# Kernel tuning notes

Hardware: AMD Instinct MI355X
Metric: run time of the kernel (lower is better)

## Reference

```python
import jax, jax.numpy as jnp
import numpy as np
from math import comb

N_INPUT, N_HIDDEN, N_LATENT = 2, 1024, 16
T, B = 320, 192
DEG = N_LATENT // 2 - 1          # 7
NPTS = DEG + 1                   # 8 control points
LAT = N_LATENT + N_LATENT // 2   # 24

_COMB = jnp.array([comb(DEG, i) for i in range(NPTS)], dtype=jnp.float32)
_I = jnp.arange(NPTS, dtype=jnp.float32)


def setup_inputs() -> dict:
    key = jax.random.key(0)
    ks = jax.random.split(key, 24)
    H = N_HIDDEN
    w = lambda k, shape, sc: (jax.random.normal(k, shape, jnp.float32) * sc)
    return dict(
        x=jax.random.normal(ks[0], (T, B, N_INPUT), jnp.float32),
        latent_ctrlpt=jax.random.normal(ks[1], (B, N_LATENT), jnp.float32),
        latent_ratw=jax.random.uniform(ks[2], (B, N_LATENT // 2), jnp.float32, 0.1, 1.0),
        # h0/c0 projection linears (forward/backward directions)
        W_hf=w(ks[3], (H, LAT), 0.2), b_hf=jnp.zeros((H,), jnp.float32),
        W_hb=w(ks[4], (H, LAT), 0.2), b_hb=jnp.zeros((H,), jnp.float32),
        W_cf=w(ks[5], (H, LAT), 0.2), b_cf=jnp.zeros((H,), jnp.float32),
        W_cb=w(ks[6], (H, LAT), 0.2), b_cb=jnp.zeros((H,), jnp.float32),
        # bi-LSTM weights, PyTorch gate order (i, f, g, o)
        W_ih_f=w(ks[7], (4 * H, N_INPUT), 0.03), W_hh_f=w(ks[8], (4 * H, H), 0.03),
        b_ih_f=jnp.zeros((4 * H,), jnp.float32), b_hh_f=jnp.zeros((4 * H,), jnp.float32),
        W_ih_b=w(ks[9], (4 * H, N_INPUT), 0.03), W_hh_b=w(ks[10], (4 * H, H), 0.03),
        b_ih_b=jnp.zeros((4 * H,), jnp.float32), b_hh_b=jnp.zeros((4 * H,), jnp.float32),
        # t-logits head
        W_log=w(ks[11], (1, 2 * H), 0.03), b_log=jnp.zeros((1,), jnp.float32),
    )


def _lstm_dir(x_tm, h0, c0, W_ih, W_hh, b_ih, b_hh, reverse):
    # x_tm: (T, B, in). Precompute input projection once (compute-efficient).
    xs = jnp.einsum('tbi,gi->tbg', x_tm, W_ih) + b_ih + b_hh  # (T, B, 4H)

    def step(carry, xt):
        h, c = carry
        g = xt + h @ W_hh.T
        i, f, gg, o = jnp.split(g, 4, axis=-1)
        c = jax.nn.sigmoid(f) * c + jax.nn.sigmoid(i) * jnp.tanh(gg)
        h = jax.nn.sigmoid(o) * jnp.tanh(c)
        return (h, c), h

    _, hs = jax.lax.scan(step, (h0, c0), xs, reverse=reverse)
    return hs  # (T, B, H)


def reference(x, latent_ctrlpt, latent_ratw,
              W_hf, b_hf, W_hb, b_hb, W_cf, b_cf, W_cb, b_cb,
              W_ih_f, W_hh_f, b_ih_f, b_hh_f,
              W_ih_b, W_hh_b, b_ih_b, b_hh_b,
              W_log, b_log):
    latent = jnp.concatenate([latent_ctrlpt, latent_ratw], axis=1)  # (B, LAT)
    h0f = jnp.tanh(latent @ W_hf.T + b_hf)
    h0b = jnp.tanh(latent @ W_hb.T + b_hb)
    c0f = jnp.tanh(latent @ W_cf.T + b_cf)
    c0b = jnp.tanh(latent @ W_cb.T + b_cb)

    hf = _lstm_dir(x, h0f, c0f, W_ih_f, W_hh_f, b_ih_f, b_hh_f, reverse=False)
    hb = _lstm_dir(x, h0b, c0b, W_ih_b, W_hh_b, b_ih_b, b_hh_b, reverse=True)
    out = jnp.concatenate([hf, hb], axis=-1)           # (T, B, 2H)
    out = jnp.transpose(out, (1, 0, 2))                # batch_first (B, T, 2H)

    logits = (out @ W_log.T + b_log)[..., 0]           # (B, T)
    ts = jnp.cumsum(jax.nn.softmax(logits, axis=1), axis=1)  # (B, T) in (0, 1]

    P = latent_ctrlpt.reshape(-1, NPTS, 2)             # (B, NPTS, 2)
    r = latent_ratw.reshape(-1, NPTS)                  # (B, NPTS)

    # Rational Bezier curve, batched over B and T (replaces per-sample loop)
    t = ts[..., None]                                   # (B, T, 1)
    basis = _COMB * t ** _I * (1.0 - t) ** (DEG - _I)   # (B, T, NPTS)
    num = basis * r[:, None, :]
    w = num / num.sum(-1, keepdims=True)
    curves = jnp.einsum('btn,bnd->btd', w, P)           # (B, T, 2)

    # mean of squared consecutive control-point distances, averaged over batch
    d2 = ((P[:, 1:, :] - P[:, :-1, :]) ** 2).sum(-1)    # (B, NPTS-1)
    reg = d2.mean()
    return curves, reg
```

## Files before the change

### kernel.cpp

```cpp
#include <hip/hip_runtime.h>
#include <stdint.h>

#define T_STEPS 320
#define BATCH   192
#define HID     1024
#define NBLK    256

typedef unsigned short u16;
typedef __bf16 bf16x8 __attribute__((ext_vector_type(8)));
typedef float  f32x4  __attribute__((ext_vector_type(4)));
typedef unsigned int u32x4 __attribute__((ext_vector_type(4)));

#define OFF_BAR      0u
#define OFF_PART     4096u
#define MEMSET_BYTES 3936256u
#define OFF_C0       3936256u
#define OFF_H        5509120u
#define OFF_WPACK    7081984u
#define OFF_COEF     23859200u
#define WS_NEED      23990272u

#define DMP_WK_STRIDE 6528
#define DMP_BYTES     104448
#define DYN_LDS       104464

__device__ __forceinline__ u16 f2bf(float f) {
  unsigned u = __float_as_uint(f);
  unsigned r = (u + 0x7FFFu + ((u >> 16) & 1u)) >> 16;
  return (u16)r;
}
__device__ __forceinline__ float sigm(float x)   { return 1.f / (1.f + __expf(-x)); }
__device__ __forceinline__ float tanh_f(float x) { return 1.f - 2.f / (1.f + __expf(2.f * x)); }

__global__ void pack_k(const float* __restrict__ Whhf, const float* __restrict__ Whhb,
                       u16* __restrict__ wpack)
{
  int lin = blockIdx.x * 256 + threadIdx.x;
  int lane = lin & 63;
  int cg   = (lin >> 6) & 3;
  int ks   = (lin >> 8) & 31;
  int jsl  = (lin >> 13) & 63;
  int dir  = (lin >> 19) & 1;
  int col  = cg * 16 + (lane & 15);
  int R    = (col & 3) * 1024 + jsl * 16 + (col >> 2);
  int kb   = ks * 32 + (lane >> 4) * 8;
  const float* W = dir ? Whhb : Whhf;
  const float* src = W + (size_t)R * 1024 + kb;
  unsigned w[4];
  #pragma unroll
  for (int e = 0; e < 4; ++e) {
    unsigned lo = f2bf(src[2 * e]);
    unsigned hi = f2bf(src[2 * e + 1]);
    w[e] = lo | (hi << 16);
  }
  *((uint4*)(wpack + (size_t)lin * 8)) = make_uint4(w[0], w[1], w[2], w[3]);
}

__global__ void coef_k(const float* __restrict__ Wihf, const float* __restrict__ bihf,
                       const float* __restrict__ bhhf,
                       const float* __restrict__ Wihb, const float* __restrict__ bihb,
                       const float* __restrict__ bhhb, float* __restrict__ coef)
{
  int id  = blockIdx.x * 256 + threadIdx.x;
  int col = id & 63;
  int jsl = (id >> 6) & 63;
  int dir = (id >> 12) & 1;
  int R   = (col & 3) * 1024 + jsl * 16 + (col >> 2);
  const float* Wih = dir ? Wihb : Wihf;
  const float* bi  = dir ? bihb : bihf;
  const float* bh  = dir ? bhhb : bhhf;
  float4 v;
  v.x = Wih[(size_t)R * 2 + 0];
  v.y = Wih[(size_t)R * 2 + 1];
  v.z = bi[R] + bh[R];
  v.w = 0.f;
  ((float4*)coef)[id] = v;
}

__global__ void init_k(const float* __restrict__ ctrl, const float* __restrict__ ratw,
                       const float* __restrict__ Whf, const float* __restrict__ bhf,
                       const float* __restrict__ Whb, const float* __restrict__ bhb,
                       const float* __restrict__ Wcf, const float* __restrict__ bcf,
                       const float* __restrict__ Wcb, const float* __restrict__ bcb,
                       u16* hb, float* c0)
{
  int idx = blockIdx.x * 256 + threadIdx.x;
  int m = blockIdx.y;
  int b = idx >> 10;
  int h = idx & 1023;
  const float* W  = (m == 0) ? Whf : (m == 1) ? Whb : (m == 2) ? Wcf : Wcb;
  const float* bi = (m == 0) ? bhf : (m == 1) ? bhb : (m == 2) ? bcf : bcb;
  float acc = bi[h];
  const float* wr = W + h * 24;
  #pragma unroll
  for (int k = 0; k < 16; ++k) acc += wr[k] * ctrl[b * 16 + k];
  #pragma unroll
  for (int k = 0; k < 8; ++k)  acc += wr[16 + k] * ratw[b * 8 + k];
  acc = tanh_f(acc);
  if (m < 2) hb[((size_t)(m * 2 + 0) * BATCH + b) * HID + h] = f2bf(acc);
  else       c0[((size_t)(m - 2) * BATCH + b) * HID + h] = acc;
}


#define ALD(S, OB) \
  asm volatile("global_load_dwordx4 %0, %1, off offset:" #OB " sc0 sc1" : "=v"(aq[S][0]) : "v"(ab0)); \
  asm volatile("global_load_dwordx4 %0, %1, off offset:" #OB " sc0 sc1" : "=v"(aq[S][1]) : "v"(ab1)); \
  asm volatile("global_load_dwordx4 %0, %1, off offset:" #OB " sc0 sc1" : "=v"(aq[S][2]) : "v"(ab2));

#define BLD(S, C) { const u16* bp_ = wb + (C) * 2048; \
  asm volatile("global_load_dwordx4 %0, %1, off offset:0"    : "=v"(bq[S][0]) : "v"(bp_)); \
  asm volatile("global_load_dwordx4 %0, %1, off offset:1024" : "=v"(bq[S][1]) : "v"(bp_)); \
  asm volatile("global_load_dwordx4 %0, %1, off offset:2048" : "=v"(bq[S][2]) : "v"(bp_)); \
  asm volatile("global_load_dwordx4 %0, %1, off offset:3072" : "=v"(bq[S][3]) : "v"(bp_)); }

#define SB __builtin_amdgcn_sched_barrier(0);

#define WB(n) \
  asm volatile("s_waitcnt vmcnt(" #n ")" ::: "memory"); \
  __builtin_amdgcn_sched_barrier(0);

#define MM(I) { \
  _Pragma("unroll") \
  for (int mt_ = 0; mt_ < 3; ++mt_) { \
    bf16x8 a_ = __builtin_bit_cast(bf16x8, aq[(I) & 3][mt_]); \
    _Pragma("unroll") \
    for (int n_ = 0; n_ < 4; ++n_) { \
      bf16x8 b_ = __builtin_bit_cast(bf16x8, bq[(I) & 3][n_]); \
      acc[mt_][n_] = __builtin_amdgcn_mfma_f32_16x16x32_bf16(a_, b_, acc[mt_][n_], 0, 0, 0); \
    } \
  } }

#define HST(PT, VL) asm volatile("global_store_short %0, %1, off sc0 sc1" :: "v"(PT), "v"(VL) : "memory")

__launch_bounds__(512, 1)
__global__ void lstm_persist(const float* __restrict__ x,
                             const float* __restrict__ wlog,
                             float* part,
                             const float* __restrict__ c0,
                             u16* hb,
                             const u16* __restrict__ wpack,
                             const float* __restrict__ coef,
                             unsigned* bar)
{
  extern __shared__ char lds[];
  float* DMP = (float*)lds;
  int* ldsflag = (int*)(lds + DMP_BYTES);

  const int tid   = threadIdx.x;
  const int bid   = blockIdx.x;
  const int dir   = bid >> 7;
  const int bhalf = (bid >> 6) & 1;
  const int jsl   = bid & 63;
  const int wave  = tid >> 6;
  const int lane  = tid & 63;
  const int wm    = wave >> 2;
  const int wk    = wave & 3;
  const int grp   = dir * 2 + bhalf;

  if (tid == 0) *ldsflag = 0;

  const int rgrp = tid >> 4;
  const int jj   = tid & 15;
  const int jglob = jsl * 16 + jj;
  float4 cf0, cf1, cf2, cf3;
  {
    const float4* cp = (const float4*)coef + ((dir * 64 + jsl) * 64 + jj * 4);
    cf0 = cp[0]; cf1 = cp[1]; cf2 = cp[2]; cf3 = cp[3];
  }
  const float wlg = wlog[dir * 1024 + jglob];

  float creg[3];
  int   bgm[3];
  #pragma unroll
  for (int mt = 0; mt < 3; ++mt) {
    int r  = rgrp * 3 + mt;
    int bg = bhalf * 96 + r;
    bgm[mt]  = bg;
    creg[mt] = c0[((size_t)dir * BATCH + bg) * HID + jglob];
  }

  const int arow0 = bhalf * 96 + wm * 48 + 0 * 16 + (lane & 15);
  const int arow1 = arow0 + 16;
  const int arow2 = arow0 + 32;
  const int koff  = wk * 256 + (lane >> 4) * 8;
  const u16* wb   = wpack + (size_t)(dir * 64 + jsl) * 65536
                          + (size_t)wk * 8 * 2048 + lane * 8;

  float* pbase = part + ((size_t)(dir * 8 + (jsl & 7)) * BATCH) * T_STEPS;

  unsigned* g1  = bar + (grp << 8) + ((jsl >> 3) << 4);
  unsigned* g2  = bar + (grp << 8) + 128;
  unsigned* rel = bar + (grp << 8) + 144;

  float* dbase = DMP + (size_t)wk * DMP_WK_STRIDE
                     + (wm * 48 + (lane >> 4) * 4) * 68 + (lane & 15);
  const int goff = rgrp * 3 * 68 + jj * 4;

  float lpv[3];
  int   lpo[3];

  __syncthreads();

  for (int s = 0; s < T_STEPS; ++s) {
    const int rbuf = s & 1;
    const u16* hsrc = hb + ((size_t)(dir * 2 + rbuf)) * BATCH * HID;
    u16*       hdst = hb + ((size_t)(dir * 2 + (rbuf ^ 1))) * BATCH * HID;
    const u16* ab0 = hsrc + (size_t)arow0 * HID + koff;
    const u16* ab1 = hsrc + (size_t)arow1 * HID + koff;
    const u16* ab2 = hsrc + (size_t)arow2 * HID + koff;

    f32x4 acc[3][4];
    #pragma unroll
    for (int mt = 0; mt < 3; ++mt)
      #pragma unroll
      for (int n = 0; n < 4; ++n)
        acc[mt][n] = (f32x4){0.f, 0.f, 0.f, 0.f};

    u32x4 aq[4][3];
    u32x4 bq[4][4];

    ALD(0, 0)   BLD(0, 0) SB
    ALD(1, 64)  BLD(1, 1) SB
    ALD(2, 128) BLD(2, 2) SB

    ALD(3, 192) BLD(3, 3) WB(21) MM(0)
    ALD(0, 256) BLD(0, 4) WB(21) MM(1)
    ALD(1, 320) BLD(1, 5) WB(21) MM(2)
    ALD(2, 384) BLD(2, 6) WB(21) MM(3)
    ALD(3, 448) BLD(3, 7) WB(21) MM(4)
                          WB(14) MM(5)
                          WB(7)  MM(6)
                          WB(0)  MM(7)

    #pragma unroll
    for (int mt = 0; mt < 3; ++mt)
      #pragma unroll
      for (int n = 0; n < 4; ++n)
        #pragma unroll
        for (int r = 0; r < 4; ++r)
          dbase[(mt * 16 + r) * 68 + n * 16] = acc[mt][n][r];
    __syncthreads();

    const int t_x = dir ? (T_STEPS - 1 - s) : s;

    #pragma unroll
    for (int mt = 0; mt < 3; ++mt) {
      const int ga = goff + mt * 68;
      f32x4 p0 = *(const f32x4*)(DMP + 0 * DMP_WK_STRIDE + ga);
      f32x4 p1 = *(const f32x4*)(DMP + 1 * DMP_WK_STRIDE + ga);
      f32x4 p2 = *(const f32x4*)(DMP + 2 * DMP_WK_STRIDE + ga);
      f32x4 p3 = *(const f32x4*)(DMP + 3 * DMP_WK_STRIDE + ga);
      f32x4 g4 = (p0 + p1) + (p2 + p3);
      int bg = bgm[mt];
      float2 xv = *(const float2*)(x + ((size_t)t_x * BATCH + bg) * 2);
      float pi = g4[0] + cf0.x * xv.x + cf0.y * xv.y + cf0.z;
      float pf = g4[1] + cf1.x * xv.x + cf1.y * xv.y + cf1.z;
      float pg = g4[2] + cf2.x * xv.x + cf2.y * xv.y + cf2.z;
      float po = g4[3] + cf3.x * xv.x + cf3.y * xv.y + cf3.z;
      float ig = sigm(pi), fg = sigm(pf), gv = tanh_f(pg), og = sigm(po);
      float c = fg * creg[mt] + ig * gv;
      creg[mt] = c;
      float h = og * tanh_f(c);
      u16* hp = hdst + (size_t)bg * HID + jglob;
      unsigned hv = (unsigned)f2bf(h);
      HST(hp, hv);
      float lp = h * wlg;
      lp += __shfl_xor(lp, 1);
      lp += __shfl_xor(lp, 2);
      lp += __shfl_xor(lp, 4);
      lp += __shfl_xor(lp, 8);
      lpv[mt] = lp;
      lpo[mt] = bg * T_STEPS + t_x;
    }

    asm volatile("s_waitcnt vmcnt(0)" ::: "memory");
    __syncthreads();

    if (jj == 0) {
      atomicAdd(&pbase[lpo[0]], lpv[0]);
      atomicAdd(&pbase[lpo[1]], lpv[1]);
      atomicAdd(&pbase[lpo[2]], lpv[2]);
    }

    if (tid == 0) {
      bool last = false;
      unsigned o1 = __hip_atomic_fetch_add(g1, 1u, __ATOMIC_RELAXED, __HIP_MEMORY_SCOPE_AGENT);
      if (o1 == (unsigned)(s * 8 + 7)) {
        unsigned o2 = __hip_atomic_fetch_add(g2, 1u, __ATOMIC_RELAXED, __HIP_MEMORY_SCOPE_AGENT);
        if (o2 == (unsigned)(s * 8 + 7)) {
          unsigned rv = (unsigned)(s + 1);
          asm volatile("global_store_dword %0, %1, off sc0 sc1" :: "v"(rel), "v"(rv) : "memory");
          last = true;
        }
      }
      if (!last) {
        long guard = 0;
        unsigned rv;
        for (;;) {
          asm volatile("global_load_dword %0, %1, off sc0 sc1" : "=v"(rv) : "v"(rel));
          asm volatile("s_waitcnt vmcnt(0)" ::: "memory");
          if ((int)rv >= s + 1) break;
          if (++guard > (1L << 20)) { *ldsflag = 1; break; }
          __builtin_amdgcn_s_sleep(2);
        }
      }
    }
    __syncthreads();
    if (*ldsflag) return;
  }
}

__global__ void post_k(const float* __restrict__ part, const float* __restrict__ ctrl,
                       const float* __restrict__ ratw, float* __restrict__ out)
{
  __shared__ float sh[T_STEPS + 64];
  const int b = blockIdx.x;
  const int t = threadIdx.x;
  float l = 0.f;
  #pragma unroll
  for (int p = 0; p < 16; ++p)
    l += part[((size_t)p * BATCH + b) * T_STEPS + t];
  sh[t] = l;
  __syncthreads();
  if (t < 64) {
    float mm = sh[t];
    for (int i = t + 64; i < T_STEPS; i += 64) mm = fmaxf(mm, sh[i]);
    #pragma unroll
    for (int o = 32; o; o >>= 1) mm = fmaxf(mm, __shfl_xor(mm, o));
    if (t == 0) sh[T_STEPS] = mm;
  }
  __syncthreads();
  const float m = sh[T_STEPS];
  float e = __expf(l - m);
  __syncthreads();
  sh[t] = e;
  __syncthreads();
  for (int off = 1; off < T_STEPS; off <<= 1) {
    float v = (t >= off) ? sh[t - off] : 0.f;
    __syncthreads();
    sh[t] += v;
    __syncthreads();
  }
  const float total = sh[T_STEPS - 1];
  const float ts = sh[t] / total;

  float px[8], py[8], rr[8];
  #pragma unroll
  for (int n = 0; n < 8; ++n) {
    px[n] = ctrl[b * 16 + 2 * n];
    py[n] = ctrl[b * 16 + 2 * n + 1];
    rr[n] = ratw[b * 8 + n];
  }
  const float C[8] = {1.f, 7.f, 21.f, 35.f, 35.f, 21.f, 7.f, 1.f};
  float tp[8], up[8];
  tp[0] = 1.f; up[0] = 1.f;
  const float u = 1.f - ts;
  #pragma unroll
  for (int n = 1; n < 8; ++n) { tp[n] = tp[n - 1] * ts; up[n] = up[n - 1] * u; }
  float den = 0.f, nx = 0.f, ny = 0.f;
  #pragma unroll
  for (int n = 0; n < 8; ++n) {
    float w = C[n] * tp[n] * up[7 - n] * rr[n];
    den += w; nx += w * px[n]; ny += w * py[n];
  }
  out[(b * T_STEPS + t) * 2 + 0] = nx / den;
  out[(b * T_STEPS + t) * 2 + 1] = ny / den;

  if (b == 0) {
    __syncthreads();
    if (t < BATCH) {
      float s2 = 0.f;
      #pragma unroll
      for (int n = 0; n < 7; ++n) {
        float dx = ctrl[t * 16 + 2 * n + 2] - ctrl[t * 16 + 2 * n + 0];
        float dy = ctrl[t * 16 + 2 * n + 3] - ctrl[t * 16 + 2 * n + 1];
        s2 += dx * dx + dy * dy;
      }
      sh[t] = s2;
    }
    __syncthreads();
    if (t == 0) {
      float tot = 0.f;
      for (int i = 0; i < BATCH; ++i) tot += sh[i];
      out[BATCH * T_STEPS * 2] = tot / (float)(BATCH * 7);
    }
  }
}

extern "C" void kernel_launch(void* const* d_in, const int* in_sizes, int n_in,
                              void* d_out, int out_size, void* d_ws, size_t ws_size,
                              hipStream_t stream)
{
  const float* x    = (const float*)d_in[0];
  const float* ctrl = (const float*)d_in[1];
  const float* ratw = (const float*)d_in[2];
  const float* Whf  = (const float*)d_in[3];
  const float* bhf  = (const float*)d_in[4];
  const float* Whb  = (const float*)d_in[5];
  const float* bhb  = (const float*)d_in[6];
  const float* Wcf  = (const float*)d_in[7];
  const float* bcf  = (const float*)d_in[8];
  const float* Wcb  = (const float*)d_in[9];
  const float* bcb  = (const float*)d_in[10];
  const float* Wihf = (const float*)d_in[11];
  const float* Whhf = (const float*)d_in[12];
  const float* bihf = (const float*)d_in[13];
  const float* bhhf = (const float*)d_in[14];
  const float* Wihb = (const float*)d_in[15];
  const float* Whhb = (const float*)d_in[16];
  const float* bihb = (const float*)d_in[17];
  const float* bhhb = (const float*)d_in[18];
  const float* Wlog = (const float*)d_in[19];
  float* out = (float*)d_out;
  char*  ws  = (char*)d_ws;
  if (ws_size < (size_t)WS_NEED) return;

  unsigned* bar    = (unsigned*)(ws + OFF_BAR);
  float*    part   = (float*)(ws + OFF_PART);
  float*    c0     = (float*)(ws + OFF_C0);
  u16*      hb     = (u16*)(ws + OFF_H);
  u16*      wpack  = (u16*)(ws + OFF_WPACK);
  float*    coef   = (float*)(ws + OFF_COEF);

  hipMemsetAsync(ws, 0, MEMSET_BYTES, stream);
  pack_k<<<4096, 256, 0, stream>>>(Whhf, Whhb, wpack);
  coef_k<<<32, 256, 0, stream>>>(Wihf, bihf, bhhf, Wihb, bihb, bhhb, coef);
  init_k<<<dim3(768, 4), 256, 0, stream>>>(ctrl, ratw, Whf, bhf, Whb, bhb,
                                           Wcf, bcf, Wcb, bcb, hb, c0);
  hipFuncSetAttribute((const void*)lstm_persist,
                      hipFuncAttributeMaxDynamicSharedMemorySize, DYN_LDS);
  lstm_persist<<<NBLK, 512, DYN_LDS, stream>>>(x, Wlog, part, c0, hb, wpack, coef, bar);
  post_k<<<BATCH, T_STEPS, 0, stream>>>(part, ctrl, ratw, out);
}
```

Before: 4.174 ms.

## Keep per-block recurrent weight slice resident in LDS across timesteps

Copies each block's 128 KB packed W_hh slice into LDS once before the time loop. Each step then reads the B operand from LDS instead of global memory, so all eight A-tile loads can be issued up front. To fit the extra LDS, the partial-sum dump buffer is shrunk and the gate epilogue now runs in four 24-row passes using 384 threads, adding several block barriers per step. This removes repeated weight traffic from global memory and L2, in exchange for extra synchronisation and more LDS pressure.

```diff
diff --git a/kernel.cpp b/kernel.cpp
--- a/kernel.cpp
+++ b/kernel.cpp
@@ -20,9 +20,9 @@
 #define OFF_COEF     23859200u
 #define WS_NEED      23990272u
 
-#define DMP_WK_STRIDE 6528
-#define DMP_BYTES     104448
-#define DYN_LDS       104464
+#define DMP_OFF_B    131072
+#define DMP_WK_STRIDE 1632
+#define DYN_LDS      157200
 
 __device__ __forceinline__ u16 f2bf(float f) {
   unsigned u = __float_as_uint(f);
@@ -107,26 +107,23 @@
   asm volatile("global_load_dwordx4 %0, %1, off offset:" #OB " sc0 sc1" : "=v"(aq[S][1]) : "v"(ab1)); \
   asm volatile("global_load_dwordx4 %0, %1, off offset:" #OB " sc0 sc1" : "=v"(aq[S][2]) : "v"(ab2));
 
-#define BLD(S, C) { const u16* bp_ = wb + (C) * 2048; \
-  asm volatile("global_load_dwordx4 %0, %1, off offset:0"    : "=v"(bq[S][0]) : "v"(bp_)); \
-  asm volatile("global_load_dwordx4 %0, %1, off offset:1024" : "=v"(bq[S][1]) : "v"(bp_)); \
-  asm volatile("global_load_dwordx4 %0, %1, off offset:2048" : "=v"(bq[S][2]) : "v"(bp_)); \
-  asm volatile("global_load_dwordx4 %0, %1, off offset:3072" : "=v"(bq[S][3]) : "v"(bp_)); }
-
-#define SB __builtin_amdgcn_sched_barrier(0);
+#define BLDS(P, C) { \
+  bv[P][0] = *(const bf16x8*)(bWl + (C) * 2048 + 0);   \
+  bv[P][1] = *(const bf16x8*)(bWl + (C) * 2048 + 512); \
+  bv[P][2] = *(const bf16x8*)(bWl + (C) * 2048 + 1024);\
+  bv[P][3] = *(const bf16x8*)(bWl + (C) * 2048 + 1536); }
 
 #define WB(n) \
   asm volatile("s_waitcnt vmcnt(" #n ")" ::: "memory"); \
   __builtin_amdgcn_sched_barrier(0);
 
-#define MM(I) { \
+#define MM(C, P) { \
   _Pragma("unroll") \
   for (int mt_ = 0; mt_ < 3; ++mt_) { \
-    bf16x8 a_ = __builtin_bit_cast(bf16x8, aq[(I) & 3][mt_]); \
+    bf16x8 a_ = __builtin_bit_cast(bf16x8, aq[C][mt_]); \
     _Pragma("unroll") \
     for (int n_ = 0; n_ < 4; ++n_) { \
-      bf16x8 b_ = __builtin_bit_cast(bf16x8, bq[(I) & 3][n_]); \
-      acc[mt_][n_] = __builtin_amdgcn_mfma_f32_16x16x32_bf16(a_, b_, acc[mt_][n_], 0, 0, 0); \
+      acc[mt_][n_] = __builtin_amdgcn_mfma_f32_16x16x32_bf16(a_, bv[P][n_], acc[mt_][n_], 0, 0, 0); \
     } \
   } }
 
@@ -143,8 +140,9 @@
                              unsigned* bar)
 {
   extern __shared__ char lds[];
-  float* DMP = (float*)lds;
-  int* ldsflag = (int*)(lds + DMP_BYTES);
+  u16*   Wlds = (u16*)lds;
+  float* DMP  = (float*)(lds + DMP_OFF_B);
+  int*   ldsflag = (int*)(lds + DMP_OFF_B + 26112);
 
   const int tid   = threadIdx.x;
   const int bid   = blockIdx.x;
@@ -156,35 +154,43 @@
   const int wm    = wave >> 2;
   const int wk    = wave & 3;
   const int grp   = dir * 2 + bhalf;
+  const int q4    = (lane >> 4) * 4;
+  const int cl    = lane & 15;
 
   if (tid == 0) *ldsflag = 0;
 
-  const int rgrp = tid >> 4;
-  const int jj   = tid & 15;
-  const int jglob = jsl * 16 + jj;
+  {
+    const uint4* wsrc = (const uint4*)wpack + (size_t)(dir * 64 + jsl) * 8192;
+    uint4* wdst = (uint4*)Wlds;
+    #pragma unroll
+    for (int i = 0; i < 16; ++i) wdst[tid + i * 512] = wsrc[tid + i * 512];
+  }
+
+  const int j    = tid & 15;
+  const int rloc = tid >> 4;
+  const bool pw  = (tid < 384);
+  const int jglob = jsl * 16 + j;
   float4 cf0, cf1, cf2, cf3;
   {
-    const float4* cp = (const float4*)coef + ((dir * 64 + jsl) * 64 + jj * 4);
+    const float4* cp = (const float4*)coef + ((dir * 64 + jsl) * 64 + j * 4);
     cf0 = cp[0]; cf1 = cp[1]; cf2 = cp[2]; cf3 = cp[3];
   }
   const float wlg = wlog[dir * 1024 + jglob];
 
-  float creg[3];
-  int   bgm[3];
-  #pragma unroll
-  for (int mt = 0; mt < 3; ++mt) {
-    int r  = rgrp * 3 + mt;
-    int bg = bhalf * 96 + r;
-    bgm[mt]  = bg;
-    creg[mt] = c0[((size_t)dir * BATCH + bg) * HID + jglob];
-  }
-
-  const int arow0 = bhalf * 96 + wm * 48 + 0 * 16 + (lane & 15);
+  float creg[4];
+  int   bgm[4];
+  #pragma unroll
+  for (int p = 0; p < 4; ++p) {
+    int bg = bhalf * 96 + p * 24 + rloc;
+    bgm[p]  = bg;
+    creg[p] = pw ? c0[((size_t)dir * BATCH + bg) * HID + jglob] : 0.f;
+  }
+
+  const int arow0 = bhalf * 96 + wm * 48 + 0 * 16 + cl;
   const int arow1 = arow0 + 16;
   const int arow2 = arow0 + 32;
   const int koff  = wk * 256 + (lane >> 4) * 8;
-  const u16* wb   = wpack + (size_t)(dir * 64 + jsl) * 65536
-                          + (size_t)wk * 8 * 2048 + lane * 8;
+  const u16* bWl  = Wlds + (size_t)wk * 16384 + lane * 8;
 
   float* pbase = part + ((size_t)(dir * 8 + (jsl & 7)) * BATCH) * T_STEPS;
 
@@ -192,12 +198,8 @@
   unsigned* g2  = bar + (grp << 8) + 128;
   unsigned* rel = bar + (grp << 8) + 144;
 
-  float* dbase = DMP + (size_t)wk * DMP_WK_STRIDE
-                     + (wm * 48 + (lane >> 4) * 4) * 68 + (lane & 15);
-  const int goff = rgrp * 3 * 68 + jj * 4;
-
-  float lpv[3];
-  int   lpo[3];
+  float lpv[4];
+  int   lpo[4];
 
   __syncthreads();
 
@@ -216,70 +218,81 @@
       for (int n = 0; n < 4; ++n)
         acc[mt][n] = (f32x4){0.f, 0.f, 0.f, 0.f};
 
-    u32x4 aq[4][3];
-    u32x4 bq[4][4];
-
-    ALD(0, 0)   BLD(0, 0) SB
-    ALD(1, 64)  BLD(1, 1) SB
-    ALD(2, 128) BLD(2, 2) SB
-
-    ALD(3, 192) BLD(3, 3) WB(21) MM(0)
-    ALD(0, 256) BLD(0, 4) WB(21) MM(1)
-    ALD(1, 320) BLD(1, 5) WB(21) MM(2)
-    ALD(2, 384) BLD(2, 6) WB(21) MM(3)
-    ALD(3, 448) BLD(3, 7) WB(21) MM(4)
-                          WB(14) MM(5)
-                          WB(7)  MM(6)
-                          WB(0)  MM(7)
+    u32x4  aq[8][3];
+    bf16x8 bv[2][4];
+
+    ALD(0, 0)   ALD(1, 64)  ALD(2, 128) ALD(3, 192)
+    ALD(4, 256) ALD(5, 320) ALD(6, 384) ALD(7, 448)
+
+    BLDS(0, 0)
+    BLDS(1, 1) WB(21) MM(0, 0)
+    BLDS(0, 2) WB(18) MM(1, 1)
+    BLDS(1, 3) WB(15) MM(2, 0)
+    BLDS(0, 4) WB(12) MM(3, 1)
+    BLDS(1, 5) WB(9)  MM(4, 0)
+    BLDS(0, 6) WB(6)  MM(5, 1)
+    BLDS(1, 7) WB(3)  MM(6, 0)
+               WB(0)  MM(7, 1)
+
+    const int t_x = dir ? (T_STEPS - 1 - s) : s;
 
     #pragma unroll
-    for (int mt = 0; mt < 3; ++mt)
-      #pragma unroll
-      for (int n = 0; n < 4; ++n)
+    for (int p = 0; p < 4; ++p) {
+      if (wm == (p >> 1)) {
+        const int plo = (p & 1) * 24;
+        float* dst = DMP + wk * DMP_WK_STRIDE;
         #pragma unroll
-        for (int r = 0; r < 4; ++r)
-          dbase[(mt * 16 + r) * 68 + n * 16] = acc[mt][n][r];
-    __syncthreads();
-
-    const int t_x = dir ? (T_STEPS - 1 - s) : s;
-
-    #pragma unroll
-    for (int mt = 0; mt < 3; ++mt) {
-      const int ga = goff + mt * 68;
-      f32x4 p0 = *(const f32x4*)(DMP + 0 * DMP_WK_STRIDE + ga);
-      f32x4 p1 = *(const f32x4*)(DMP + 1 * DMP_WK_STRIDE + ga);
-      f32x4 p2 = *(const f32x4*)(DMP + 2 * DMP_WK_STRIDE + ga);
-      f32x4 p3 = *(const f32x4*)(DMP + 3 * DMP_WK_STRIDE + ga);
-      f32x4 g4 = (p0 + p1) + (p2 + p3);
-      int bg = bgm[mt];
-      float2 xv = *(const float2*)(x + ((size_t)t_x * BATCH + bg) * 2);
-      float pi = g4[0] + cf0.x * xv.x + cf0.y * xv.y + cf0.z;
-      float pf = g4[1] + cf1.x * xv.x + cf1.y * xv.y + cf1.z;
-      float pg = g4[2] + cf2.x * xv.x + cf2.y * xv.y + cf2.z;
-      float po = g4[3] + cf3.x * xv.x + cf3.y * xv.y + cf3.z;
-      float ig = sigm(pi), fg = sigm(pf), gv = tanh_f(pg), og = sigm(po);
-      float c = fg * creg[mt] + ig * gv;
-      creg[mt] = c;
-      float h = og * tanh_f(c);
-      u16* hp = hdst + (size_t)bg * HID + jglob;
-      unsigned hv = (unsigned)f2bf(h);
-      HST(hp, hv);
-      float lp = h * wlg;
-      lp += __shfl_xor(lp, 1);
-      lp += __shfl_xor(lp, 2);
-      lp += __shfl_xor(lp, 4);
-      lp += __shfl_xor(lp, 8);
-      lpv[mt] = lp;
-      lpo[mt] = bg * T_STEPS + t_x;
+        for (int mt = 0; mt < 3; ++mt)
+          #pragma unroll
+          for (int n = 0; n < 4; ++n)
+            #pragma unroll
+            for (int r = 0; r < 4; ++r) {
+              int row = mt * 16 + q4 + r;
+              if (row >= plo && row < plo + 24)
+                dst[(row - plo) * 68 + n * 16 + cl] = acc[mt][n][r];
+            }
+      }
+      __syncthreads();
+
+      if (pw) {
+        const int ga = rloc * 68 + (j >> 2) * 16 + (j & 3) * 4;
+        f32x4 p0 = *(const f32x4*)(DMP + 0 * DMP_WK_STRIDE + ga);
+        f32x4 p1 = *(const f32x4*)(DMP + 1 * DMP_WK_STRIDE + ga);
+        f32x4 p2 = *(const f32x4*)(DMP + 2 * DMP_WK_STRIDE + ga);
+        f32x4 p3 = *(const f32x4*)(DMP + 3 * DMP_WK_STRIDE + ga);
+        f32x4 g4 = (p0 + p1) + (p2 + p3);
+        int bg = bgm[p];
+        float2 xv = *(const float2*)(x + ((size_t)t_x * BATCH + bg) * 2);
+        float pi = g4[0] + cf0.x * xv.x + cf0.y * xv.y + cf0.z;
+        float pf = g4[1] + cf1.x * xv.x + cf1.y * xv.y + cf1.z;
+        float pg = g4[2] + cf2.x * xv.x + cf2.y * xv.y + cf2.z;
+        float po = g4[3] + cf3.x * xv.x + cf3.y * xv.y + cf3.z;
+        float ig = sigm(pi), fg = sigm(pf), gv = tanh_f(pg), og = sigm(po);
+        float c = fg * creg[p] + ig * gv;
+        creg[p] = c;
+        float h = og * tanh_f(c);
+        u16* hp = hdst + (size_t)bg * HID + jglob;
+        unsigned hv = (unsigned)f2bf(h);
+        HST(hp, hv);
+        float lp = h * wlg;
+        lp += __shfl_xor(lp, 1);
+        lp += __shfl_xor(lp, 2);
+        lp += __shfl_xor(lp, 4);
+        lp += __shfl_xor(lp, 8);
+        lpv[p] = lp;
+        lpo[p] = bg * T_STEPS + t_x;
+      }
+      __syncthreads();
     }
 
     asm volatile("s_waitcnt vmcnt(0)" ::: "memory");
     __syncthreads();
 
-    if (jj == 0) {
+    if (pw && j == 0) {
       atomicAdd(&pbase[lpo[0]], lpv[0]);
       atomicAdd(&pbase[lpo[1]], lpv[1]);
       atomicAdd(&pbase[lpo[2]], lpv[2]);
+      atomicAdd(&pbase[lpo[3]], lpv[3]);
     }
 
     if (tid == 0) {
```

After: 4.016 ms. 1.04x faster.
